# Performance work log

Hardware: AMD Instinct MI355X
Metric: run time of the kernel (lower is better)

## Reference

```python
import jax, jax.numpy as jnp
import numpy as np

N_USERS = 50000
N_ENTITIES = 100000
D = 64
R = 16
E_UI = 1500000
E_KG = 100000


def setup_inputs() -> dict:
    key = jax.random.key(0)
    ks = jax.random.split(key, 7)
    s = 1.0 / np.sqrt(D)  # ~xavier scale
    return {
        "user_indices": jnp.arange(N_USERS, dtype=jnp.int32),
        "item_indices": jnp.arange(N_ENTITIES, dtype=jnp.int32),
        "edge_index_ui": jax.random.randint(ks[0], (2, E_UI), 0, N_USERS + N_ENTITIES, dtype=jnp.int32),
        "edge_index_kg": jax.random.randint(ks[1], (2, E_KG), 0, N_ENTITIES, dtype=jnp.int32),
        "edge_type_kg": jax.random.randint(ks[2], (E_KG,), 0, R, dtype=jnp.int32),
        "user_table": (jax.random.normal(ks[3], (N_USERS, D)) * s).astype(jnp.float32),
        "entity_table": (jax.random.normal(ks[4], (N_ENTITIES, D)) * s).astype(jnp.float32),
        "W": (jax.random.normal(ks[5], (D, D)) * s).astype(jnp.float32),
        "W_r": (jax.random.normal(ks[6], (R, D, D)) * s).astype(jnp.float32),
    }


def _kgat_layer(x, edge_index, W, W_r, edge_type=None):
    # PyG aggr='add', flow source_to_target: x_j = x[src], x_i = x[dst], scatter to dst
    src, dst = edge_index[0], edge_index[1]
    x_j = x[src]  # [E, D]
    x_i = x[dst]  # [E, D]
    if edge_type is None:
        x_j_t = x_j @ W  # [E, D]
    else:
        # per-edge relation-specific transform: bmm(x_j[:,None,:], W_r[edge_type])
        x_j_t = jnp.einsum('ed,edo->eo', x_j, W_r[edge_type])
    # bi-interaction attention
    x_i_t = x_i @ W
    logits = jnp.sum(x_i_t * x_j_t, axis=1, keepdims=True)  # [E, 1]
    logits = jax.nn.leaky_relu(logits, negative_slope=0.2)
    scores = jax.nn.softmax(logits, axis=0)  # GLOBAL softmax over all edges (as in source)
    msg = scores * x_j_t  # [E, D]
    return jax.ops.segment_sum(msg, dst, num_segments=x.shape[0])


def reference(user_indices, item_indices, edge_index_ui, edge_index_kg, edge_type_kg,
              user_table, entity_table, W, W_r):
    user_embeds = user_table[user_indices]      # [n_users, D]
    item_embeds = entity_table[item_indices]    # [n_entities, D]
    x = jnp.concatenate([user_embeds, item_embeds], axis=0)
    # single layer (layer_dims = [embed_dim])
    x_ui = _kgat_layer(x, edge_index_ui, W, W_r, edge_type=None)
    x_kg = _kgat_layer(item_embeds, edge_index_kg, W, W_r, edge_type=edge_type_kg)
    x = x.at[N_USERS:].add(x_kg)  # faithful to source: overwritten by next line (dead store)
    x = jax.nn.relu(x_ui)
    # F.dropout(training=False) -> identity in eval mode
    return (x[:N_USERS], x[N_USERS:])
```

## Files before the change

### kernel.cpp

```cpp
#include <hip/hip_runtime.h>

#define NU 50000
#define NE 100000
#define NN 150000
#define DD 64
#define EUI 1500000

#define TPB 256
#define NBLK 2048
#define NXB 2344
#define NXH (NXB + NBLK)
#define NBF2 9375
#define NSC 9375

#define XWB_OFF    0ull
#define CNT_OFF    4800000ull
#define PSUM_OFF   4950000ull
#define SCAL_OFF   4959375ull

__device__ __forceinline__ unsigned bfpack(float a, float b) {
  unsigned ua = __float_as_uint(a);
  ua = (ua + 0x7fffu + ((ua >> 16) & 1u)) >> 16;
  unsigned ub = __float_as_uint(b);
  ub = (ub + 0x7fffu + ((ub >> 16) & 1u)) & 0xffff0000u;
  return (ua & 0xffffu) | ub;
}

template <int CTRL>
__device__ __forceinline__ float dpp_add(float x) {
  int y = __builtin_amdgcn_update_dpp(0, __float_as_int(x), CTRL, 0xF, 0xF, false);
  return x + __int_as_float(y);
}
__device__ __forceinline__ float row16_sum(float x) {
  x = dpp_add<0x124>(x);
  x = dpp_add<0x128>(x);
  x = dpp_add<0xB1>(x);
  x = dpp_add<0x4E>(x);
  return x;
}

__global__ __launch_bounds__(TPB) void k_xw_hist(const int* __restrict__ uidx,
                                                 const int* __restrict__ iidx,
                                                 const float* __restrict__ ut,
                                                 const float* __restrict__ et,
                                                 const float* __restrict__ W,
                                                 unsigned* __restrict__ xwb,
                                                 const int* __restrict__ ei,
                                                 unsigned* __restrict__ cnt,
                                                 int* __restrict__ ssrcp) {
  const int bi = blockIdx.x;
  int idx;
  bool hist;
  if (bi < 2 * NBLK) { hist = (bi & 1); idx = bi >> 1; }
  else               { hist = false;    idx = bi - NBLK; }

  if (hist) {
    for (int e = idx * TPB + threadIdx.x; e < EUI; e += NBLK * TPB) {
      const int dst = ei[EUI + e];
      const int src = ei[e];
      const unsigned r = atomicAdd(&cnt[dst], 1u);
      if (r < 64u) ssrcp[((size_t)dst << 6) + r] = src;
    }
    return;
  }

  __shared__ float Ws[DD * DD];
  __shared__ float Xs[64 * 68];
  const int t = threadIdx.x;
  {
    const float4* W4 = (const float4*)W;
    float4* Ws4 = (float4*)Ws;
#pragma unroll
    for (int i = 0; i < 4; ++i) Ws4[t + i * TPB] = W4[t + i * TPB];
  }
  {
    const int rl = t >> 2, ch = t & 3;
    int row = idx * 64 + rl;
    if (row >= NN) row = NN - 1;
    const float4* s4 = (const float4*)((row < NU)
        ? ut + (size_t)uidx[row] * DD
        : et + (size_t)iidx[row - NU] * DD);
    float4* x4 = (float4*)(Xs + rl * 68);
#pragma unroll
    for (int j = 0; j < 4; ++j) x4[ch + 4 * j] = s4[ch + 4 * j];
  }
  __syncthreads();
  const int q = t & 15, g = t >> 4;
  float4 acc[4] = {{0,0,0,0},{0,0,0,0},{0,0,0,0},{0,0,0,0}};
  const float* __restrict__ wsq = Ws + 4 * q;
  const float* __restrict__ xsg = Xs + (4 * g) * 68;
#pragma unroll 1
  for (int kc = 0; kc < 16; ++kc) {
    const float4 w0 = *(const float4*)(wsq + (4 * kc + 0) * DD);
    const float4 w1 = *(const float4*)(wsq + (4 * kc + 1) * DD);
    const float4 w2 = *(const float4*)(wsq + (4 * kc + 2) * DD);
    const float4 w3 = *(const float4*)(wsq + (4 * kc + 3) * DD);
#pragma unroll
    for (int i = 0; i < 4; ++i) {
      const float4 x = *(const float4*)(xsg + i * 68 + 4 * kc);
      acc[i].x = fmaf(x.x, w0.x, acc[i].x);
      acc[i].y = fmaf(x.x, w0.y, acc[i].y);
      acc[i].z = fmaf(x.x, w0.z, acc[i].z);
      acc[i].w = fmaf(x.x, w0.w, acc[i].w);
      acc[i].x = fmaf(x.y, w1.x, acc[i].x);
      acc[i].y = fmaf(x.y, w1.y, acc[i].y);
      acc[i].z = fmaf(x.y, w1.z, acc[i].z);
      acc[i].w = fmaf(x.y, w1.w, acc[i].w);
      acc[i].x = fmaf(x.z, w2.x, acc[i].x);
      acc[i].y = fmaf(x.z, w2.y, acc[i].y);
      acc[i].z = fmaf(x.z, w2.z, acc[i].z);
      acc[i].w = fmaf(x.z, w2.w, acc[i].w);
      acc[i].x = fmaf(x.w, w3.x, acc[i].x);
      acc[i].y = fmaf(x.w, w3.y, acc[i].y);
      acc[i].z = fmaf(x.w, w3.z, acc[i].z);
      acc[i].w = fmaf(x.w, w3.w, acc[i].w);
    }
  }
#pragma unroll
  for (int i = 0; i < 4; ++i) {
    const int row = idx * 64 + 4 * g + i;
    if (row < NN) {
      uint2 p;
      p.x = bfpack(acc[i].x, acc[i].y);
      p.y = bfpack(acc[i].z, acc[i].w);
      ((uint2*)(xwb + (size_t)row * 32))[q] = p;
    }
  }
}

__global__ __launch_bounds__(TPB) void k_fused(const unsigned* __restrict__ cnt,
                                               const int* ssrcp,
                                               const unsigned* __restrict__ xwb,
                                               float* out,
                                               float* __restrict__ psum) {
  const int lane = threadIdx.x & 63;
  const int wv = threadIdx.x >> 6;
  const int sub = lane >> 4;
  const int q = lane & 15;
  const int n = blockIdx.x * 16 + wv * 4 + sub;
  const uint2* __restrict__ x2 = (const uint2*)xwb;
  const uint2 dv = x2[(size_t)n * 16 + q];
  const float vd0 = __uint_as_float(dv.x << 16);
  const float vd1 = __uint_as_float(dv.x & 0xffff0000u);
  const float vd2 = __uint_as_float(dv.y << 16);
  const float vd3 = __uint_as_float(dv.y & 0xffff0000u);
  const int deg = min((int)cnt[n], 64);
  int dmax = deg;
  dmax = max(dmax, __shfl_xor(dmax, 16, 64));
  dmax = max(dmax, __shfl_xor(dmax, 32, 64));
  const size_t base = (size_t)n << 6;
  const int nit = (dmax + 3) >> 2;
  float a0 = 0.f, a1 = 0.f, a2 = 0.f, a3 = 0.f, wacc = 0.f;
  int sl0 = ssrcp[base], sl1 = ssrcp[base + 1];
  int sl2 = ssrcp[base + 2], sl3 = ssrcp[base + 3];
  for (int ii = 0; ii < nit; ++ii) {
    const int it = 4 * ii;
    int s0 = sl0, s1 = sl1, s2 = sl2, s3 = sl3;
    if (ii + 1 < nit) {
      sl0 = ssrcp[base + it + 4];
      sl1 = ssrcp[base + it + 5];
      sl2 = ssrcp[base + it + 6];
      sl3 = ssrcp[base + it + 7];
    }
    const bool act0 = it < deg;
    const bool act1 = it + 1 < deg;
    const bool act2 = it + 2 < deg;
    const bool act3 = it + 3 < deg;
    if (!act0) s0 = 0;
    if (!act1) s1 = 0;
    if (!act2) s2 = 0;
    if (!act3) s3 = 0;
    const uint2 sv0 = x2[(size_t)s0 * 16 + q];
    const uint2 sv1 = x2[(size_t)s1 * 16 + q];
    const uint2 sv2 = x2[(size_t)s2 * 16 + q];
    const uint2 sv3 = x2[(size_t)s3 * 16 + q];
    const float u0 = __uint_as_float(sv0.x << 16);
    const float u1 = __uint_as_float(sv0.x & 0xffff0000u);
    const float u2 = __uint_as_float(sv0.y << 16);
    const float u3 = __uint_as_float(sv0.y & 0xffff0000u);
    const float t0 = __uint_as_float(sv1.x << 16);
    const float t1 = __uint_as_float(sv1.x & 0xffff0000u);
    const float t2 = __uint_as_float(sv1.y << 16);
    const float t3 = __uint_as_float(sv1.y & 0xffff0000u);
    const float g0 = __uint_as_float(sv2.x << 16);
    const float g1 = __uint_as_float(sv2.x & 0xffff0000u);
    const float g2 = __uint_as_float(sv2.y << 16);
    const float g3 = __uint_as_float(sv2.y & 0xffff0000u);
    const float h0 = __uint_as_float(sv3.x << 16);
    const float h1 = __uint_as_float(sv3.x & 0xffff0000u);
    const float h2 = __uint_as_float(sv3.y << 16);
    const float h3 = __uint_as_float(sv3.y & 0xffff0000u);
    float p0 = vd0 * u0;
    p0 = fmaf(vd1, u1, p0); p0 = fmaf(vd2, u2, p0); p0 = fmaf(vd3, u3, p0);
    float p1 = vd0 * t0;
    p1 = fmaf(vd1, t1, p1); p1 = fmaf(vd2, t2, p1); p1 = fmaf(vd3, t3, p1);
    float p2 = vd0 * g0;
    p2 = fmaf(vd1, g1, p2); p2 = fmaf(vd2, g2, p2); p2 = fmaf(vd3, g3, p2);
    float p3 = vd0 * h0;
    p3 = fmaf(vd1, h1, p3); p3 = fmaf(vd2, h2, p3); p3 = fmaf(vd3, h3, p3);
    p0 = row16_sum(p0);
    p1 = row16_sum(p1);
    p2 = row16_sum(p2);
    p3 = row16_sum(p3);
    const float l0 = (p0 > 0.f) ? p0 : 0.2f * p0;
    const float l1 = (p1 > 0.f) ? p1 : 0.2f * p1;
    const float l2 = (p2 > 0.f) ? p2 : 0.2f * p2;
    const float l3 = (p3 > 0.f) ? p3 : 0.2f * p3;
    float w0 = __expf(l0);
    float w1 = __expf(l1);
    float w2 = __expf(l2);
    float w3 = __expf(l3);
    if (!act0) w0 = 0.f;
    if (!act1) w1 = 0.f;
    if (!act2) w2 = 0.f;
    if (!act3) w3 = 0.f;
    a0 = fmaf(w0, u0, a0); a1 = fmaf(w0, u1, a1);
    a2 = fmaf(w0, u2, a2); a3 = fmaf(w0, u3, a3);
    a0 = fmaf(w1, t0, a0); a1 = fmaf(w1, t1, a1);
    a2 = fmaf(w1, t2, a2); a3 = fmaf(w1, t3, a3);
    a0 = fmaf(w2, g0, a0); a1 = fmaf(w2, g1, a1);
    a2 = fmaf(w2, g2, a2); a3 = fmaf(w2, g3, a3);
    a0 = fmaf(w3, h0, a0); a1 = fmaf(w3, h1, a1);
    a2 = fmaf(w3, h2, a2); a3 = fmaf(w3, h3, a3);
    wacc += (w0 + w1) + (w2 + w3);
  }
  float4 r = {a0, a1, a2, a3};
  ((float4*)(out + (size_t)n * DD))[q] = r;
  __shared__ float sm[16];
  if (q == 0) sm[wv * 4 + sub] = wacc;
  __syncthreads();
  if (threadIdx.x == 0) {
    float s = 0.f;
#pragma unroll
    for (int i = 0; i < 16; ++i) s += sm[i];
    psum[blockIdx.x] = s;
  }
}

__global__ __launch_bounds__(TPB) void k_rsum(const float* __restrict__ psum,
                                              float* __restrict__ scal) {
  float s = 0.f;
  for (int i = threadIdx.x; i < NBF2; i += TPB) s += psum[i];
#pragma unroll
  for (int off = 32; off; off >>= 1) s += __shfl_xor(s, off, 64);
  __shared__ float sm[4];
  if ((threadIdx.x & 63) == 0) sm[threadIdx.x >> 6] = s;
  __syncthreads();
  if (threadIdx.x == 0) scal[0] = sm[0] + sm[1] + sm[2] + sm[3];
}

__global__ __launch_bounds__(TPB) void k_scale(float* __restrict__ out,
                                               const float* __restrict__ scal) {
  const float inv = 1.0f / scal[0];
  const int i = blockIdx.x * TPB + threadIdx.x;
  float4* o4 = (float4*)out;
  float4 v = o4[i];
  v.x = fmaxf(v.x * inv, 0.f);
  v.y = fmaxf(v.y * inv, 0.f);
  v.z = fmaxf(v.z * inv, 0.f);
  v.w = fmaxf(v.w * inv, 0.f);
  o4[i] = v;
}

extern "C" void kernel_launch(void* const* d_in, const int* in_sizes, int n_in,
                              void* d_out, int out_size, void* d_ws, size_t ws_size,
                              hipStream_t stream) {
  const int* uidx = (const int*)d_in[0];
  const int* iidx = (const int*)d_in[1];
  const int* ei_ui = (const int*)d_in[2];
  const float* ut = (const float*)d_in[5];
  const float* et = (const float*)d_in[6];
  const float* W = (const float*)d_in[7];

  float* out = (float*)d_out;
  float* ws = (float*)d_ws;
  unsigned* xwb = (unsigned*)(ws + XWB_OFF);
  unsigned* cnt = (unsigned*)(ws + CNT_OFF);
  float* psum = ws + PSUM_OFF;
  float* scal = ws + SCAL_OFF;
  int* ssrcp = (int*)d_out;

  (void)hipMemsetAsync(cnt, 0, (size_t)NN * sizeof(unsigned), stream);

  k_xw_hist<<<NXH, TPB, 0, stream>>>(uidx, iidx, ut, et, W, xwb, ei_ui, cnt, ssrcp);
  k_fused<<<NBF2, TPB, 0, stream>>>(cnt, ssrcp, xwb, out, psum);
  k_rsum<<<1, TPB, 0, stream>>>(psum, scal);
  k_scale<<<NSC, TPB, 0, stream>>>(out, scal);
}
```

Baseline: 261.1 us.

## Gather neighbors from 7-bit block-quantized XW copy and fold reduction into atomics

Adds a second copy of the transformed embeddings packed as four 7-bit signed values plus a shared 4-bit power-of-two exponent per 32-bit word. The edge gather loop reads this copy, halving the bytes fetched per neighbor compared with bf16, and applies the scale to both the logit and the message. It also drops the separate reduction kernel: each block atomically adds its weight sum into a scalar that is zeroed by an enlarged memset. The cost is much lower precision for source embeddings, which may exceed tolerance, plus an extra write pass in the XW kernel and float atomic contention on a single address.

Result: slower. 705.3 us (+170.1%).

```diff
diff --git a/kernel.cpp b/kernel.cpp
--- a/kernel.cpp
+++ b/kernel.cpp
@@ -15,8 +15,8 @@
 
 #define XWB_OFF    0ull
 #define CNT_OFF    4800000ull
-#define PSUM_OFF   4950000ull
-#define SCAL_OFF   4959375ull
+#define SCAL_OFF   4950000ull
+#define XWQ_OFF    4950004ull
 
 __device__ __forceinline__ unsigned bfpack(float a, float b) {
   unsigned ua = __float_as_uint(a);
@@ -26,6 +26,32 @@
   return (ua & 0xffffu) | ub;
 }
 
+__device__ __forceinline__ unsigned q7pack4(float a, float b, float c, float d) {
+  const float m = fmaxf(fmaxf(fabsf(a), fabsf(b)), fmaxf(fabsf(c), fabsf(d)));
+  int E = -20;
+  if (m >= 3.0517578125e-05f) {
+    E = (int)((__float_as_uint(m) >> 23) & 0xffu) - 132;
+    E = max(-20, min(-5, E));
+  }
+  const float s = __uint_as_float((unsigned)(127 - E) << 23);
+  const int qa = max(-64, min(63, (int)rintf(a * s)));
+  const int qb = max(-64, min(63, (int)rintf(b * s)));
+  const int qc = max(-64, min(63, (int)rintf(c * s)));
+  const int qd = max(-64, min(63, (int)rintf(d * s)));
+  return ((unsigned)(E + 20) << 28) |
+         (unsigned)(qa & 0x7f) | ((unsigned)(qb & 0x7f) << 7) |
+         ((unsigned)(qc & 0x7f) << 14) | ((unsigned)(qd & 0x7f) << 21);
+}
+
+__device__ __forceinline__ void q7unpack4(unsigned v, float& s, float& a,
+                                          float& b, float& c, float& d) {
+  s = __uint_as_float(((v >> 28) + 107u) << 23);
+  a = (float)((int)(v << 25) >> 25);
+  b = (float)((int)(v << 18) >> 25);
+  c = (float)((int)(v << 11) >> 25);
+  d = (float)((int)(v << 4) >> 25);
+}
+
 template <int CTRL>
 __device__ __forceinline__ float dpp_add(float x) {
   int y = __builtin_amdgcn_update_dpp(0, __float_as_int(x), CTRL, 0xF, 0xF, false);
@@ -45,6 +71,7 @@
                                                  const float* __restrict__ et,
                                                  const float* __restrict__ W,
                                                  unsigned* __restrict__ xwb,
+                                                 unsigned* __restrict__ xwq,
                                                  const int* __restrict__ ei,
                                                  unsigned* __restrict__ cnt,
                                                  int* __restrict__ ssrcp) {
@@ -124,6 +151,7 @@
       p.x = bfpack(acc[i].x, acc[i].y);
       p.y = bfpack(acc[i].z, acc[i].w);
       ((uint2*)(xwb + (size_t)row * 32))[q] = p;
+      xwq[(size_t)row * 16 + q] = q7pack4(acc[i].x, acc[i].y, acc[i].z, acc[i].w);
     }
   }
 }
@@ -131,8 +159,9 @@
 __global__ __launch_bounds__(TPB) void k_fused(const unsigned* __restrict__ cnt,
                                                const int* ssrcp,
                                                const unsigned* __restrict__ xwb,
+                                               const unsigned* __restrict__ xwq,
                                                float* out,
-                                               float* __restrict__ psum) {
+                                               float* __restrict__ scal) {
   const int lane = threadIdx.x & 63;
   const int wv = threadIdx.x >> 6;
   const int sub = lane >> 4;
@@ -170,26 +199,18 @@
     if (!act1) s1 = 0;
     if (!act2) s2 = 0;
     if (!act3) s3 = 0;
-    const uint2 sv0 = x2[(size_t)s0 * 16 + q];
-    const uint2 sv1 = x2[(size_t)s1 * 16 + q];
-    const uint2 sv2 = x2[(size_t)s2 * 16 + q];
-    const uint2 sv3 = x2[(size_t)s3 * 16 + q];
-    const float u0 = __uint_as_float(sv0.x << 16);
-    const float u1 = __uint_as_float(sv0.x & 0xffff0000u);
-    const float u2 = __uint_as_float(sv0.y << 16);
-    const float u3 = __uint_as_float(sv0.y & 0xffff0000u);
-    const float t0 = __uint_as_float(sv1.x << 16);
-    const float t1 = __uint_as_float(sv1.x & 0xffff0000u);
-    const float t2 = __uint_as_float(sv1.y << 16);
-    const float t3 = __uint_as_float(sv1.y & 0xffff0000u);
-    const float g0 = __uint_as_float(sv2.x << 16);
-    const float g1 = __uint_as_float(sv2.x & 0xffff0000u);
-    const float g2 = __uint_as_float(sv2.y << 16);
-    const float g3 = __uint_as_float(sv2.y & 0xffff0000u);
-    const float h0 = __uint_as_float(sv3.x << 16);
-    const float h1 = __uint_as_float(sv3.x & 0xffff0000u);
-    const float h2 = __uint_as_float(sv3.y << 16);
-    const float h3 = __uint_as_float(sv3.y & 0xffff0000u);
+    const unsigned sv0 = xwq[(size_t)s0 * 16 + q];
+    const unsigned sv1 = xwq[(size_t)s1 * 16 + q];
+    const unsigned sv2 = xwq[(size_t)s2 * 16 + q];
+    const unsigned sv3 = xwq[(size_t)s3 * 16 + q];
+    float se0, u0, u1, u2, u3;
+    float se1, t0, t1, t2, t3;
+    float se2, g0, g1, g2, g3;
+    float se3, h0, h1, h2, h3;
+    q7unpack4(sv0, se0, u0, u1, u2, u3);
+    q7unpack4(sv1, se1, t0, t1, t2, t3);
+    q7unpack4(sv2, se2, g0, g1, g2, g3);
+    q7unpack4(sv3, se3, h0, h1, h2, h3);
     float p0 = vd0 * u0;
     p0 = fmaf(vd1, u1, p0); p0 = fmaf(vd2, u2, p0); p0 = fmaf(vd3, u3, p0);
     float p1 = vd0 * t0;
@@ -198,6 +219,10 @@
     p2 = fmaf(vd1, g1, p2); p2 = fmaf(vd2, g2, p2); p2 = fmaf(vd3, g3, p2);
     float p3 = vd0 * h0;
     p3 = fmaf(vd1, h1, p3); p3 = fmaf(vd2, h2, p3); p3 = fmaf(vd3, h3, p3);
+    p0 *= se0;
+    p1 *= se1;
+    p2 *= se2;
+    p3 *= se3;
     p0 = row16_sum(p0);
     p1 = row16_sum(p1);
     p2 = row16_sum(p2);
@@ -214,14 +239,18 @@
     if (!act1) w1 = 0.f;
     if (!act2) w2 = 0.f;
     if (!act3) w3 = 0.f;
-    a0 = fmaf(w0, u0, a0); a1 = fmaf(w0, u1, a1);
-    a2 = fmaf(w0, u2, a2); a3 = fmaf(w0, u3, a3);
-    a0 = fmaf(w1, t0, a0); a1 = fmaf(w1, t1, a1);
-    a2 = fmaf(w1, t2, a2); a3 = fmaf(w1, t3, a3);
-    a0 = fmaf(w2, g0, a0); a1 = fmaf(w2, g1, a1);
-    a2 = fmaf(w2, g2, a2); a3 = fmaf(w2, g3, a3);
-    a0 = fmaf(w3, h0, a0); a1 = fmaf(w3, h1, a1);
-    a2 = fmaf(w3, h2, a2); a3 = fmaf(w3, h3, a3);
+    const float ws0 = w0 * se0;
+    const float ws1 = w1 * se1;
+    const float ws2 = w2 * se2;
+    const float ws3 = w3 * se3;
+    a0 = fmaf(ws0, u0, a0); a1 = fmaf(ws0, u1, a1);
+    a2 = fmaf(ws0, u2, a2); a3 = fmaf(ws0, u3, a3);
+    a0 = fmaf(ws1, t0, a0); a1 = fmaf(ws1, t1, a1);
+    a2 = fmaf(ws1, t2, a2); a3 = fmaf(ws1, t3, a3);
+    a0 = fmaf(ws2, g0, a0); a1 = fmaf(ws2, g1, a1);
+    a2 = fmaf(ws2, g2, a2); a3 = fmaf(ws2, g3, a3);
+    a0 = fmaf(ws3, h0, a0); a1 = fmaf(ws3, h1, a1);
+    a2 = fmaf(ws3, h2, a2); a3 = fmaf(ws3, h3, a3);
     wacc += (w0 + w1) + (w2 + w3);
   }
   float4 r = {a0, a1, a2, a3};
@@ -233,20 +262,8 @@
     float s = 0.f;
 #pragma unroll
     for (int i = 0; i < 16; ++i) s += sm[i];
-    psum[blockIdx.x] = s;
-  }
-}
-
-__global__ __launch_bounds__(TPB) void k_rsum(const float* __restrict__ psum,
-                                              float* __restrict__ scal) {
-  float s = 0.f;
-  for (int i = threadIdx.x; i < NBF2; i += TPB) s += psum[i];
-#pragma unroll
-  for (int off = 32; off; off >>= 1) s += __shfl_xor(s, off, 64);
-  __shared__ float sm[4];
-  if ((threadIdx.x & 63) == 0) sm[threadIdx.x >> 6] = s;
-  __syncthreads();
-  if (threadIdx.x == 0) scal[0] = sm[0] + sm[1] + sm[2] + sm[3];
+    atomicAdd(scal, s);
+  }
 }
 
 __global__ __launch_bounds__(TPB) void k_scale(float* __restrict__ out,
@@ -276,14 +293,14 @@
   float* ws = (float*)d_ws;
   unsigned* xwb = (unsigned*)(ws + XWB_OFF);
   unsigned* cnt = (unsigned*)(ws + CNT_OFF);
-  float* psum = ws + PSUM_OFF;
   float* scal = ws + SCAL_OFF;
+  unsigned* xwq = (unsigned*)(ws + XWQ_OFF);
   int* ssrcp = (int*)d_out;
 
-  (void)hipMemsetAsync(cnt, 0, (size_t)NN * sizeof(unsigned), stream);
-
-  k_xw_hist<<<NXH, TPB, 0, stream>>>(uidx, iidx, ut, et, W, xwb, ei_ui, cnt, ssrcp);
-  k_fused<<<NBF2, TPB, 0, stream>>>(cnt, ssrcp, xwb, out, psum);
-  k_rsum<<<1, TPB, 0, stream>>>(psum, scal);
+  (void)hipMemsetAsync(cnt, 0, (size_t)(NN + 1) * sizeof(unsigned), stream);
+
+  k_xw_hist<<<NXH, TPB, 0, stream>>>(uidx, iidx, ut, et, W, xwb, xwq, ei_ui,
+                                     cnt, ssrcp);
+  k_fused<<<NBF2, TPB, 0, stream>>>(cnt, ssrcp, xwb, xwq, out, scal);
   k_scale<<<NSC, TPB, 0, stream>>>(out, scal);
 }
```
